# Performance work log

Hardware: AMD Instinct MI355X
Metric: run time of the kernel (lower is better)

Reference implementation:

```python
import jax, jax.numpy as jnp
import numpy as np

N = 100000
E = 1600000
D_IN = 128
D_HID = 128
D_OUT = 64


def mish(x):
    return x * jnp.tanh(jax.nn.softplus(x))


def sage_conv(x, src, dst, W_l, b_l, W_r):
    # gather source-node features along edges, mean-aggregate at destination
    msg = x[src]  # [E, d]
    agg = jax.ops.segment_sum(msg, dst, num_segments=N)  # [N, d]
    cnt = jax.ops.segment_sum(jnp.ones((E,), x.dtype), dst, num_segments=N)
    agg = agg / jnp.maximum(cnt, 1.0)[:, None]
    # PyG SAGEConv: lin_l(aggregated) + lin_r(root); lin_r has no bias
    return agg @ W_l.T + b_l + x @ W_r.T


def setup_inputs() -> dict:
    key = jax.random.key(0)
    ks = jax.random.split(key, 10)
    s = lambda d: 1.0 / np.sqrt(d)
    return {
        "x": jax.random.normal(ks[0], (N, D_IN), jnp.float32),
        "edge_index": jax.random.randint(ks[1], (2, E), 0, N, jnp.int64),
        "W_l0": jax.random.normal(ks[2], (D_HID, D_IN), jnp.float32) * s(D_IN),
        "b_l0": jnp.zeros((D_HID,), jnp.float32),
        "W_r0": jax.random.normal(ks[3], (D_HID, D_IN), jnp.float32) * s(D_IN),
        "W_l1": jax.random.normal(ks[4], (D_HID, D_HID), jnp.float32) * s(D_HID),
        "b_l1": jnp.zeros((D_HID,), jnp.float32),
        "W_r1": jax.random.normal(ks[5], (D_HID, D_HID), jnp.float32) * s(D_HID),
        "W_head": jax.random.normal(ks[6], (D_OUT, D_HID), jnp.float32) * s(D_HID),
        "b_head": jnp.zeros((D_OUT,), jnp.float32),
    }


def reference(x, edge_index, W_l0, b_l0, W_r0, W_l1, b_l1, W_r1, W_head, b_head):
    src, dst = edge_index[0], edge_index[1]
    h = mish(sage_conv(x, src, dst, W_l0, b_l0, W_r0))  # dropout is identity in eval
    h = mish(sage_conv(h, src, dst, W_l1, b_l1, W_r1))
    return h @ W_head.T + b_head
```

## Files before the change

### kernel.cpp

```cpp
#include <hip/hip_runtime.h>
#include <math.h>

#define N_NODES 100000
#define N_EDGES 1600000
#define DF      128
#define D_HEAD  64

#define NWIN    128
#define WIN_SZ  782
#define CAP     13312
#define BCH     8192

typedef __attribute__((ext_vector_type(8))) short bf16x8;
typedef __attribute__((ext_vector_type(4))) float f32x4;

static __device__ __forceinline__ float mish_f(float v) {
    float e = __expf(v);
    float q = 1.0f + e;
    float p = q * q;
    float m = v * (p - 1.0f) / (p + 1.0f);
    return (v > 40.0f) ? v : m;
}

static __device__ __forceinline__ unsigned short f2bf(float f) {
    unsigned int u = __builtin_bit_cast(unsigned int, f);
    unsigned int r = (u + 0x7fffu + ((u >> 16) & 1u)) >> 16;
    return (unsigned short)r;
}
static __device__ __forceinline__ float bf2f(unsigned int bits16) {
    return __builtin_bit_cast(float, bits16 << 16);
}


#define XB 12500
#define WB 288

__global__ void cvt_kernel(const float* __restrict__ x,
                           const float* __restrict__ Wl0, const float* __restrict__ Wr0,
                           const float* __restrict__ Wl1, const float* __restrict__ Wr1,
                           const float* __restrict__ Wh,
                           unsigned short* __restrict__ xb, unsigned short* __restrict__ wb,
                           int* __restrict__ bucket_cnt) {
    int b = blockIdx.x;
    if (b < XB) {
        int i = b * 256 + threadIdx.x;
        float4 v = ((const float4*)x)[i];
        ushort4 o;
        o.x = f2bf(v.x); o.y = f2bf(v.y); o.z = f2bf(v.z); o.w = f2bf(v.w);
        ((ushort4*)xb)[i] = o;
    } else if (b < XB + WB) {
        int id = (b - XB) * 256 + threadIdx.x;
        if (id < 65536) {
            int seg = id >> 14;
            int r   = id & 16383;
            const float* W = (seg == 0) ? Wl0 : (seg == 1) ? Wr0 : (seg == 2) ? Wl1 : Wr1;
            wb[id] = f2bf(W[r]);
        } else {
            wb[id] = f2bf(Wh[id - 65536]);
        }
    } else {
        if (threadIdx.x < NWIN) bucket_cnt[threadIdx.x] = 0;
    }
}


__global__ __launch_bounds__(256) void bucket_kernel(const int* __restrict__ src,
                                                     const int* __restrict__ dst,
                                                     int* __restrict__ bucket_cnt,
                                                     unsigned int* __restrict__ pairs) {
    __shared__ int cnt[NWIN];
    __shared__ int base[NWIN];
    int tid = threadIdx.x;
    int e0  = blockIdx.x * BCH;
    if (tid < NWIN) cnt[tid] = 0;
    __syncthreads();
    #pragma unroll 4
    for (int i = 0; i < BCH / 256; ++i) {
        int e = e0 + tid + i * 256;
        if (e < N_EDGES) atomicAdd(&cnt[dst[e] / WIN_SZ], 1);
    }
    __syncthreads();
    if (tid < NWIN) {
        base[tid] = atomicAdd(&bucket_cnt[tid], cnt[tid]);
        cnt[tid] = 0;
    }
    __syncthreads();
    #pragma unroll 4
    for (int i = 0; i < BCH / 256; ++i) {
        int e = e0 + tid + i * 256;
        if (e < N_EDGES) {
            int d  = dst[e];
            int s  = src[e];
            int w  = d / WIN_SZ;
            int dl = d - w * WIN_SZ;
            int p  = atomicAdd(&cnt[w], 1);
            int idx = base[w] + p;
            if (idx < CAP)
                pairs[(size_t)w * CAP + idx] = (unsigned)s | ((unsigned)dl << 17);
        }
    }
}


__global__ __launch_bounds__(256) void build_win(const unsigned int* __restrict__ pairs,
                                                 const int* __restrict__ bucket_cnt,
                                                 int* __restrict__ rowstart,
                                                 int* __restrict__ csr) {
    __shared__ int ldeg[WIN_SZ];
    __shared__ int lcsr[CAP];
    __shared__ int wsum[4];
    __shared__ int red[4];

    int tid = threadIdx.x;
    int w   = blockIdx.x;
    int base_node = w * WIN_SZ;
    int nn = N_NODES - base_node;
    if (nn > WIN_SZ) nn = WIN_SZ;
    if (nn < 0) nn = 0;

    for (int i = tid; i < WIN_SZ; i += 256) ldeg[i] = 0;

    int val = (tid < w) ? bucket_cnt[tid] : 0;
    #pragma unroll
    for (int o = 32; o; o >>= 1) val += __shfl_xor(val, o);
    if ((tid & 63) == 0) red[tid >> 6] = val;
    int n_pairs = bucket_cnt[w];
    if (n_pairs > CAP) n_pairs = CAP;
    __syncthreads();
    int ebase = red[0] + red[1] + red[2] + red[3];

    const unsigned int* pw = pairs + (size_t)w * CAP;

    for (int i = tid; i < n_pairs; i += 256)
        atomicAdd(&ldeg[pw[i] >> 17], 1);
    __syncthreads();

    int i0 = tid * 4;
    int v[4];
    int s = 0;
    #pragma unroll
    for (int q = 0; q < 4; ++q) {
        v[q] = (i0 + q < nn) ? ldeg[i0 + q] : 0;
        s += v[q];
    }
    int lane = tid & 63, wv = tid >> 6;
    int sc = s;
    #pragma unroll
    for (int d = 1; d < 64; d <<= 1) {
        int t = __shfl_up(sc, d);
        if (lane >= d) sc += t;
    }
    if (lane == 63) wsum[wv] = sc;
    __syncthreads();
    int woff = 0;
    for (int q = 0; q < wv; ++q) woff += wsum[q];
    int run = woff + sc - s;
    #pragma unroll
    for (int q = 0; q < 4; ++q) {
        if (i0 + q < nn) {
            rowstart[base_node + i0 + q] = ebase + run;
            ldeg[i0 + q] = run;
            run += v[q];
        }
    }
    if (w == NWIN - 1 && tid == 0) rowstart[N_NODES] = N_EDGES;
    __syncthreads();

    for (int i = tid; i < n_pairs; i += 256) {
        unsigned int p = pw[i];
        int slot = atomicAdd(&ldeg[p >> 17], 1);
        lcsr[slot] = (int)(p & 0x1FFFFu);
    }
    __syncthreads();

    for (int i = tid; i < n_pairs; i += 256)
        csr[ebase + i] = lcsr[i];
}


__global__ __launch_bounds__(256) void aggregate_kernel(const unsigned short* __restrict__ X,
                                                        const int* __restrict__ rowstart,
                                                        const int* __restrict__ csr,
                                                        unsigned short* __restrict__ out) {
    int wv   = threadIdx.x >> 6;
    int lane = threadIdx.x & 63;
    int node = blockIdx.x * 4 + wv;
    if (node >= N_NODES) return;
    int slot = lane >> 4;
    int l16  = lane & 15;
    int rs0 = rowstart[node];
    int rs1 = rowstart[node + 1];

    float acc[8];
    #pragma unroll
    for (int i = 0; i < 8; ++i) acc[i] = 0.f;

    for (int e0 = rs0; e0 < rs1; e0 += 16) {
        uint4 v[4];
        #pragma unroll
        for (int j = 0; j < 4; ++j) {
            int e = e0 + 4 * j + slot;
            uint4 t = {0u, 0u, 0u, 0u};
            if (e < rs1) t = *(const uint4*)(X + (size_t)csr[e] * DF + l16 * 8);
            v[j] = t;
        }
        #pragma unroll
        for (int j = 0; j < 4; ++j) {
            unsigned int w0[4] = {v[j].x, v[j].y, v[j].z, v[j].w};
            #pragma unroll
            for (int i = 0; i < 4; ++i) {
                acc[2 * i]     += bf2f(w0[i] & 0xffffu);
                acc[2 * i + 1] += bf2f(w0[i] >> 16);
            }
        }
    }

    #pragma unroll
    for (int i = 0; i < 8; ++i) {
        acc[i] += __shfl_xor(acc[i], 32);
        acc[i] += __shfl_xor(acc[i], 16);
    }

    int d = rs1 - rs0;
    float inv = 1.0f / (float)(d > 0 ? d : 1);
    if (slot == 0) {
        unsigned int r[4];
        #pragma unroll
        for (int i = 0; i < 4; ++i) {
            unsigned int lo = f2bf(acc[2 * i] * inv);
            unsigned int hi = f2bf(acc[2 * i + 1] * inv);
            r[i] = lo | (hi << 16);
        }
        uint4 o = {r[0], r[1], r[2], r[3]};
        *(uint4*)(out + (size_t)node * DF + l16 * 8) = o;
    }
}


template <int COLS, bool TWO, bool MISH, bool OUT_BF16>
__global__ __launch_bounds__(256) void mfma_gemm(const unsigned short* __restrict__ A,
                                                 const unsigned short* __restrict__ H,
                                                 const unsigned short* __restrict__ Wl,
                                                 const unsigned short* __restrict__ Wr,
                                                 const float* __restrict__ bias,
                                                 void* __restrict__ out, int M) {
    constexpr int NT  = COLS / 16;
    constexpr int LDA = 136;

    __shared__ unsigned short As[64 * LDA];
    __shared__ unsigned short Ws[COLS * LDA];

    int tid  = threadIdx.x;
    int wv   = tid >> 6;
    int lane = tid & 63;
    int quad = lane >> 4;
    int l16  = lane & 15;
    int m0   = blockIdx.x * 64;

    f32x4 acc[NT];
    #pragma unroll
    for (int n = 0; n < NT; ++n) acc[n] = (f32x4){0.f, 0.f, 0.f, 0.f};

    #pragma unroll
    for (int phase = 0; phase < (TWO ? 2 : 1); ++phase) {
        const unsigned short* Ain = phase ? H : A;
        const unsigned short* Win = phase ? Wr : Wl;
        __syncthreads();
        #pragma unroll
        for (int i = 0; i < COLS / 16; ++i) {
            int idx = tid + i * 256;
            int r   = idx >> 4;
            int cb  = (idx & 15) * 8;
            *(uint4*)&Ws[r * LDA + cb] = *(const uint4*)&Win[r * 128 + cb];
        }
        #pragma unroll
        for (int i = 0; i < 4; ++i) {
            int idx = tid + i * 256;
            int r   = idx >> 4;
            int cb  = (idx & 15) * 8;
            uint4 v = {0u, 0u, 0u, 0u};
            if (m0 + r < M) v = *(const uint4*)&Ain[(size_t)(m0 + r) * 128 + cb];
            *(uint4*)&As[r * LDA + cb] = v;
        }
        __syncthreads();
        #pragma unroll
        for (int ks = 0; ks < 4; ++ks) {
            bf16x8 af = *(const bf16x8*)&As[(wv * 16 + l16) * LDA + ks * 32 + quad * 8];
            #pragma unroll
            for (int n = 0; n < NT; ++n) {
                bf16x8 bfr = *(const bf16x8*)&Ws[(n * 16 + l16) * LDA + ks * 32 + quad * 8];
                acc[n] = __builtin_amdgcn_mfma_f32_16x16x32_bf16(af, bfr, acc[n], 0, 0, 0);
            }
        }
    }

    #pragma unroll
    for (int n = 0; n < NT; ++n) {
        int col = n * 16 + l16;
        float b = bias[col];
        #pragma unroll
        for (int r = 0; r < 4; ++r) {
            int row = m0 + wv * 16 + quad * 4 + r;
            if (row < M) {
                float v = acc[n][r] + b;
                if constexpr (MISH) v = mish_f(v);
                if constexpr (OUT_BF16)
                    ((unsigned short*)out)[(size_t)row * COLS + col] = f2bf(v);
                else
                    ((float*)out)[(size_t)row * COLS + col] = v;
            }
        }
    }
}


extern "C" void kernel_launch(void* const* d_in, const int* in_sizes, int n_in,
                              void* d_out, int out_size, void* d_ws, size_t ws_size,
                              hipStream_t stream) {
    const float* x   = (const float*)d_in[0];
    const int*   ei  = (const int*)d_in[1];
    const float* Wl0 = (const float*)d_in[2];
    const float* bl0 = (const float*)d_in[3];
    const float* Wr0 = (const float*)d_in[4];
    const float* Wl1 = (const float*)d_in[5];
    const float* bl1 = (const float*)d_in[6];
    const float* Wr1 = (const float*)d_in[7];
    const float* Wh  = (const float*)d_in[8];
    const float* bh  = (const float*)d_in[9];
    float* out = (float*)d_out;

    const int* src = ei;
    const int* dst = ei + N_EDGES;

    char* ws = (char*)d_ws;
    size_t off = 0;
    auto alloc = [&](size_t bytes) -> void* {
        void* p = ws + off;
        off += (bytes + 255) & ~(size_t)255;
        return p;
    };
    int* rowstart   = (int*)alloc((N_NODES + 1) * 4);
    int* csr        = (int*)alloc(N_EDGES * 4);
    int* bucket_cnt = (int*)alloc(NWIN * 4);

    unsigned short* Wb  = (unsigned short*)alloc((size_t)(65536 + 8192) * 2);
    unsigned short* Xb  = (unsigned short*)alloc((size_t)N_NODES * DF * 2);
    unsigned short* Ab  = (unsigned short*)alloc((size_t)N_NODES * DF * 2);
    unsigned short* H1b = (unsigned short*)alloc((size_t)N_NODES * DF * 2);

    unsigned short* Wlb0 = Wb;
    unsigned short* Wrb0 = Wb + 16384;
    unsigned short* Wlb1 = Wb + 32768;
    unsigned short* Wrb1 = Wb + 49152;
    unsigned short* Whb  = Wb + 65536;
    unsigned short* H2b  = Xb;
    unsigned int* pairs  = (unsigned int*)H1b;

    cvt_kernel<<<XB + WB + 1, 256, 0, stream>>>(x, Wl0, Wr0, Wl1, Wr1, Wh, Xb, Wb, bucket_cnt);

    bucket_kernel<<<(N_EDGES + BCH - 1) / BCH, 256, 0, stream>>>(src, dst, bucket_cnt, pairs);
    build_win<<<NWIN, 256, 0, stream>>>(pairs, bucket_cnt, rowstart, csr);

    const int gemm_grid = (N_NODES + 63) / 64;

    aggregate_kernel<<<N_NODES / 4, 256, 0, stream>>>(Xb, rowstart, csr, Ab);
    mfma_gemm<128, true, true, true><<<gemm_grid, 256, 0, stream>>>(
        Ab, Xb, Wlb0, Wrb0, bl0, H1b, N_NODES);
    aggregate_kernel<<<N_NODES / 4, 256, 0, stream>>>(H1b, rowstart, csr, Ab);
    mfma_gemm<128, true, true, true><<<gemm_grid, 256, 0, stream>>>(
        Ab, H1b, Wlb1, Wrb1, bl1, H2b, N_NODES);
    mfma_gemm<64, false, false, false><<<gemm_grid, 256, 0, stream>>>(
        H2b, nullptr, Whb, nullptr, bh, out, N_NODES);
}
```

Measured before the change: 381.0 us.

## Fuse neighbor aggregation into SAGE GEMM and split bucket atomics

Each wave now mean-aggregates its 16 destination nodes straight into shared memory. It then runs the Wl MFMA from there, reloads the root rows into the same tile for the Wr MFMA, and applies bias and mish in the same kernel. This removes the separate aggregation kernel and the global write and read of the aggregated matrix for both layers. Weights are now read from global/cache rather than staged in LDS, and each wave walks its nodes one after another. The edge-bucketing kernel also spreads each window counter over 4 per-lane-set sub-counters to cut shared-memory atomic contention.

```diff
diff --git a/kernel.cpp b/kernel.cpp
--- a/kernel.cpp
+++ b/kernel.cpp
@@ -68,21 +68,26 @@
                                                      const int* __restrict__ dst,
                                                      int* __restrict__ bucket_cnt,
                                                      unsigned int* __restrict__ pairs) {
-    __shared__ int cnt[NWIN];
-    __shared__ int base[NWIN];
+    __shared__ int cnt[NWIN][4];
+    __shared__ int cur[NWIN][4];
     int tid = threadIdx.x;
+    int set = tid & 3;
     int e0  = blockIdx.x * BCH;
-    if (tid < NWIN) cnt[tid] = 0;
+    for (int i = tid; i < NWIN * 4; i += 256) ((int*)cnt)[i] = 0;
     __syncthreads();
     #pragma unroll 4
     for (int i = 0; i < BCH / 256; ++i) {
         int e = e0 + tid + i * 256;
-        if (e < N_EDGES) atomicAdd(&cnt[dst[e] / WIN_SZ], 1);
+        if (e < N_EDGES) atomicAdd(&cnt[dst[e] / WIN_SZ][set], 1);
     }
     __syncthreads();
     if (tid < NWIN) {
-        base[tid] = atomicAdd(&bucket_cnt[tid], cnt[tid]);
-        cnt[tid] = 0;
+        int c0 = cnt[tid][0], c1 = cnt[tid][1], c2 = cnt[tid][2], c3 = cnt[tid][3];
+        int b = atomicAdd(&bucket_cnt[tid], c0 + c1 + c2 + c3);
+        cur[tid][0] = b;
+        cur[tid][1] = b + c0;
+        cur[tid][2] = b + c0 + c1;
+        cur[tid][3] = b + c0 + c1 + c2;
     }
     __syncthreads();
     #pragma unroll 4
@@ -93,8 +98,7 @@
             int s  = src[e];
             int w  = d / WIN_SZ;
             int dl = d - w * WIN_SZ;
-            int p  = atomicAdd(&cnt[w], 1);
-            int idx = base[w] + p;
+            int idx = atomicAdd(&cur[w][set], 1);
             if (idx < CAP)
                 pairs[(size_t)w * CAP + idx] = (unsigned)s | ((unsigned)dl << 17);
         }
@@ -178,77 +182,15 @@
 }
 
 
-__global__ __launch_bounds__(256) void aggregate_kernel(const unsigned short* __restrict__ X,
-                                                        const int* __restrict__ rowstart,
-                                                        const int* __restrict__ csr,
-                                                        unsigned short* __restrict__ out) {
-    int wv   = threadIdx.x >> 6;
-    int lane = threadIdx.x & 63;
-    int node = blockIdx.x * 4 + wv;
-    if (node >= N_NODES) return;
-    int slot = lane >> 4;
-    int l16  = lane & 15;
-    int rs0 = rowstart[node];
-    int rs1 = rowstart[node + 1];
-
-    float acc[8];
-    #pragma unroll
-    for (int i = 0; i < 8; ++i) acc[i] = 0.f;
-
-    for (int e0 = rs0; e0 < rs1; e0 += 16) {
-        uint4 v[4];
-        #pragma unroll
-        for (int j = 0; j < 4; ++j) {
-            int e = e0 + 4 * j + slot;
-            uint4 t = {0u, 0u, 0u, 0u};
-            if (e < rs1) t = *(const uint4*)(X + (size_t)csr[e] * DF + l16 * 8);
-            v[j] = t;
-        }
-        #pragma unroll
-        for (int j = 0; j < 4; ++j) {
-            unsigned int w0[4] = {v[j].x, v[j].y, v[j].z, v[j].w};
-            #pragma unroll
-            for (int i = 0; i < 4; ++i) {
-                acc[2 * i]     += bf2f(w0[i] & 0xffffu);
-                acc[2 * i + 1] += bf2f(w0[i] >> 16);
-            }
-        }
-    }
-
-    #pragma unroll
-    for (int i = 0; i < 8; ++i) {
-        acc[i] += __shfl_xor(acc[i], 32);
-        acc[i] += __shfl_xor(acc[i], 16);
-    }
-
-    int d = rs1 - rs0;
-    float inv = 1.0f / (float)(d > 0 ? d : 1);
-    if (slot == 0) {
-        unsigned int r[4];
-        #pragma unroll
-        for (int i = 0; i < 4; ++i) {
-            unsigned int lo = f2bf(acc[2 * i] * inv);
-            unsigned int hi = f2bf(acc[2 * i + 1] * inv);
-            r[i] = lo | (hi << 16);
-        }
-        uint4 o = {r[0], r[1], r[2], r[3]};
-        *(uint4*)(out + (size_t)node * DF + l16 * 8) = o;
-    }
-}
-
-
-template <int COLS, bool TWO, bool MISH, bool OUT_BF16>
-__global__ __launch_bounds__(256) void mfma_gemm(const unsigned short* __restrict__ A,
-                                                 const unsigned short* __restrict__ H,
-                                                 const unsigned short* __restrict__ Wl,
-                                                 const unsigned short* __restrict__ Wr,
-                                                 const float* __restrict__ bias,
-                                                 void* __restrict__ out, int M) {
-    constexpr int NT  = COLS / 16;
+__global__ __launch_bounds__(256, 4) void fused_sage(const unsigned short* __restrict__ X,
+                                                     const int* __restrict__ rowstart,
+                                                     const int* __restrict__ csr,
+                                                     const unsigned short* __restrict__ Wl,
+                                                     const unsigned short* __restrict__ Wr,
+                                                     const float* __restrict__ bias,
+                                                     unsigned short* __restrict__ out) {
     constexpr int LDA = 136;
-
     __shared__ unsigned short As[64 * LDA];
-    __shared__ unsigned short Ws[COLS * LDA];
 
     int tid  = threadIdx.x;
     int wv   = tid >> 6;
@@ -257,58 +199,147 @@
     int l16  = lane & 15;
     int m0   = blockIdx.x * 64;
 
-    f32x4 acc[NT];
-    #pragma unroll
-    for (int n = 0; n < NT; ++n) acc[n] = (f32x4){0.f, 0.f, 0.f, 0.f};
-
-    #pragma unroll
-    for (int phase = 0; phase < (TWO ? 2 : 1); ++phase) {
-        const unsigned short* Ain = phase ? H : A;
-        const unsigned short* Win = phase ? Wr : Wl;
-        __syncthreads();
-        #pragma unroll
-        for (int i = 0; i < COLS / 16; ++i) {
-            int idx = tid + i * 256;
-            int r   = idx >> 4;
-            int cb  = (idx & 15) * 8;
-            *(uint4*)&Ws[r * LDA + cb] = *(const uint4*)&Win[r * 128 + cb];
-        }
-        #pragma unroll
-        for (int i = 0; i < 4; ++i) {
-            int idx = tid + i * 256;
-            int r   = idx >> 4;
-            int cb  = (idx & 15) * 8;
-            uint4 v = {0u, 0u, 0u, 0u};
-            if (m0 + r < M) v = *(const uint4*)&Ain[(size_t)(m0 + r) * 128 + cb];
-            *(uint4*)&As[r * LDA + cb] = v;
-        }
-        __syncthreads();
-        #pragma unroll
-        for (int ks = 0; ks < 4; ++ks) {
-            bf16x8 af = *(const bf16x8*)&As[(wv * 16 + l16) * LDA + ks * 32 + quad * 8];
+    for (int n = 0; n < 16; ++n) {
+        int node = m0 + wv * 16 + n;
+        float acc[8];
+        #pragma unroll
+        for (int i = 0; i < 8; ++i) acc[i] = 0.f;
+        int rs0 = 0, rs1 = 0;
+        if (node < N_NODES) { rs0 = rowstart[node]; rs1 = rowstart[node + 1]; }
+        for (int e0 = rs0; e0 < rs1; e0 += 16) {
+            uint4 v[4];
             #pragma unroll
-            for (int n = 0; n < NT; ++n) {
-                bf16x8 bfr = *(const bf16x8*)&Ws[(n * 16 + l16) * LDA + ks * 32 + quad * 8];
-                acc[n] = __builtin_amdgcn_mfma_f32_16x16x32_bf16(af, bfr, acc[n], 0, 0, 0);
+            for (int j = 0; j < 4; ++j) {
+                int e = e0 + 4 * j + quad;
+                uint4 t = {0u, 0u, 0u, 0u};
+                if (e < rs1) t = *(const uint4*)(X + (size_t)csr[e] * DF + l16 * 8);
+                v[j] = t;
             }
-        }
-    }
-
-    #pragma unroll
-    for (int n = 0; n < NT; ++n) {
+            #pragma unroll
+            for (int j = 0; j < 4; ++j) {
+                unsigned int w0[4] = {v[j].x, v[j].y, v[j].z, v[j].w};
+                #pragma unroll
+                for (int i = 0; i < 4; ++i) {
+                    acc[2 * i]     += bf2f(w0[i] & 0xffffu);
+                    acc[2 * i + 1] += bf2f(w0[i] >> 16);
+                }
+            }
+        }
+        #pragma unroll
+        for (int i = 0; i < 8; ++i) {
+            acc[i] += __shfl_xor(acc[i], 32);
+            acc[i] += __shfl_xor(acc[i], 16);
+        }
+        if (quad == 0) {
+            int dcnt = rs1 - rs0;
+            float inv = 1.0f / (float)(dcnt > 0 ? dcnt : 1);
+            unsigned int r[4];
+            #pragma unroll
+            for (int i = 0; i < 4; ++i) {
+                unsigned int lo = f2bf(acc[2 * i] * inv);
+                unsigned int hi = f2bf(acc[2 * i + 1] * inv);
+                r[i] = lo | (hi << 16);
+            }
+            uint4 o = {r[0], r[1], r[2], r[3]};
+            *(uint4*)&As[(wv * 16 + n) * LDA + l16 * 8] = o;
+        }
+    }
+
+    f32x4 acc[8];
+    #pragma unroll
+    for (int n = 0; n < 8; ++n) acc[n] = (f32x4){0.f, 0.f, 0.f, 0.f};
+    #pragma unroll
+    for (int ks = 0; ks < 4; ++ks) {
+        bf16x8 af = *(const bf16x8*)&As[(wv * 16 + l16) * LDA + ks * 32 + quad * 8];
+        #pragma unroll
+        for (int n = 0; n < 8; ++n) {
+            bf16x8 bfr = *(const bf16x8*)&Wl[(n * 16 + l16) * 128 + ks * 32 + quad * 8];
+            acc[n] = __builtin_amdgcn_mfma_f32_16x16x32_bf16(af, bfr, acc[n], 0, 0, 0);
+        }
+    }
+
+    #pragma unroll
+    for (int i = 0; i < 4; ++i) {
+        int o   = i * 1024 + lane * 16;
+        int row = o >> 8;
+        int col = o & 255;
+        int gr  = m0 + wv * 16 + row;
+        if (gr > N_NODES - 1) gr = N_NODES - 1;
+        uint4 t = *(const uint4*)((const char*)X + (size_t)gr * 256 + col);
+        *(uint4*)((char*)As + (size_t)(wv * 16 + row) * (LDA * 2) + col) = t;
+    }
+
+    #pragma unroll
+    for (int ks = 0; ks < 4; ++ks) {
+        bf16x8 af = *(const bf16x8*)&As[(wv * 16 + l16) * LDA + ks * 32 + quad * 8];
+        #pragma unroll
+        for (int n = 0; n < 8; ++n) {
+            bf16x8 bfr = *(const bf16x8*)&Wr[(n * 16 + l16) * 128 + ks * 32 + quad * 8];
+            acc[n] = __builtin_amdgcn_mfma_f32_16x16x32_bf16(af, bfr, acc[n], 0, 0, 0);
+        }
+    }
+
+    #pragma unroll
+    for (int n = 0; n < 8; ++n) {
         int col = n * 16 + l16;
         float b = bias[col];
         #pragma unroll
         for (int r = 0; r < 4; ++r) {
             int row = m0 + wv * 16 + quad * 4 + r;
-            if (row < M) {
-                float v = acc[n][r] + b;
-                if constexpr (MISH) v = mish_f(v);
-                if constexpr (OUT_BF16)
-                    ((unsigned short*)out)[(size_t)row * COLS + col] = f2bf(v);
-                else
-                    ((float*)out)[(size_t)row * COLS + col] = v;
+            if (row < N_NODES) {
+                float v = mish_f(acc[n][r] + b);
+                out[(size_t)row * 128 + col] = f2bf(v);
             }
+        }
+    }
+}
+
+
+__global__ __launch_bounds__(256, 4) void head_gemm(const unsigned short* __restrict__ H,
+                                                    const unsigned short* __restrict__ Wh,
+                                                    const float* __restrict__ bias,
+                                                    float* __restrict__ out) {
+    constexpr int LDA = 136;
+    __shared__ unsigned short As[64 * LDA];
+    int tid  = threadIdx.x;
+    int wv   = tid >> 6;
+    int lane = tid & 63;
+    int quad = lane >> 4;
+    int l16  = lane & 15;
+    int m0   = blockIdx.x * 64;
+
+    #pragma unroll
+    for (int i = 0; i < 4; ++i) {
+        int o   = i * 1024 + lane * 16;
+        int row = o >> 8;
+        int col = o & 255;
+        int gr  = m0 + wv * 16 + row;
+        if (gr > N_NODES - 1) gr = N_NODES - 1;
+        uint4 t = *(const uint4*)((const char*)H + (size_t)gr * 256 + col);
+        *(uint4*)((char*)As + (size_t)(wv * 16 + row) * (LDA * 2) + col) = t;
+    }
+
+    f32x4 acc[4];
+    #pragma unroll
+    for (int n = 0; n < 4; ++n) acc[n] = (f32x4){0.f, 0.f, 0.f, 0.f};
+    #pragma unroll
+    for (int ks = 0; ks < 4; ++ks) {
+        bf16x8 af = *(const bf16x8*)&As[(wv * 16 + l16) * LDA + ks * 32 + quad * 8];
+        #pragma unroll
+        for (int n = 0; n < 4; ++n) {
+            bf16x8 bfr = *(const bf16x8*)&Wh[(n * 16 + l16) * 128 + ks * 32 + quad * 8];
+            acc[n] = __builtin_amdgcn_mfma_f32_16x16x32_bf16(af, bfr, acc[n], 0, 0, 0);
+        }
+    }
+
+    #pragma unroll
+    for (int n = 0; n < 4; ++n) {
+        int col = n * 16 + l16;
+        float b = bias[col];
+        #pragma unroll
+        for (int r = 0; r < 4; ++r) {
+            int row = m0 + wv * 16 + quad * 4 + r;
+            if (row < N_NODES) out[(size_t)row * 64 + col] = acc[n][r] + b;
         }
     }
 }
@@ -345,7 +376,6 @@
 
     unsigned short* Wb  = (unsigned short*)alloc((size_t)(65536 + 8192) * 2);
     unsigned short* Xb  = (unsigned short*)alloc((size_t)N_NODES * DF * 2);
-    unsigned short* Ab  = (unsigned short*)alloc((size_t)N_NODES * DF * 2);
     unsigned short* H1b = (unsigned short*)alloc((size_t)N_NODES * DF * 2);
 
     unsigned short* Wlb0 = Wb;
@@ -361,14 +391,9 @@
     bucket_kernel<<<(N_EDGES + BCH - 1) / BCH, 256, 0, stream>>>(src, dst, bucket_cnt, pairs);
     build_win<<<NWIN, 256, 0, stream>>>(pairs, bucket_cnt, rowstart, csr);
 
-    const int gemm_grid = (N_NODES + 63) / 64;
-
-    aggregate_kernel<<<N_NODES / 4, 256, 0, stream>>>(Xb, rowstart, csr, Ab);
-    mfma_gemm<128, true, true, true><<<gemm_grid, 256, 0, stream>>>(
-        Ab, Xb, Wlb0, Wrb0, bl0, H1b, N_NODES);
-    aggregate_kernel<<<N_NODES / 4, 256, 0, stream>>>(H1b, rowstart, csr, Ab);
-    mfma_gemm<128, true, true, true><<<gemm_grid, 256, 0, stream>>>(
-        Ab, H1b, Wlb1, Wrb1, bl1, H2b, N_NODES);
-    mfma_gemm<64, false, false, false><<<gemm_grid, 256, 0, stream>>>(
-        H2b, nullptr, Whb, nullptr, bh, out, N_NODES);
-}
+    const int grid = (N_NODES + 63) / 64;
+
+    fused_sage<<<grid, 256, 0, stream>>>(Xb,  rowstart, csr, Wlb0, Wrb0, bl0, H1b);
+    fused_sage<<<grid, 256, 0, stream>>>(H1b, rowstart, csr, Wlb1, Wrb1, bl1, H2b);
+    head_gemm<<<grid, 256, 0, stream>>>(H2b, Whb, bh, out);
+}
```

New measurement: 496.5 us. 1.3x slower.

## Load GEMM operands directly from global memory and split bucket counters by lane set

Applied to the files above, without the earlier changes.

The GEMM kernels no longer stage activations and weights through shared memory. Each wave loads its A fragments and its weight fragments straight from global memory, which removes the LDS round trips and the block barriers, raises the occupancy hint, and clamps tail rows instead of zero-filling them. The bucketing kernel spreads its shared-memory counters over four sub-counters per window to cut atomic contention, and it keeps the dst values in registers so dst is not read twice. The cost is that weight fragments are now re-read from global memory or cache by every wave.

```diff
diff --git a/kernel.cpp b/kernel.cpp
--- a/kernel.cpp
+++ b/kernel.cpp
@@ -68,33 +68,41 @@
                                                      const int* __restrict__ dst,
                                                      int* __restrict__ bucket_cnt,
                                                      unsigned int* __restrict__ pairs) {
-    __shared__ int cnt[NWIN];
-    __shared__ int base[NWIN];
+    __shared__ int cnt[NWIN][4];
+    __shared__ int cur[NWIN][4];
     int tid = threadIdx.x;
+    int set = tid & 3;
     int e0  = blockIdx.x * BCH;
-    if (tid < NWIN) cnt[tid] = 0;
-    __syncthreads();
+    for (int i = tid; i < NWIN * 4; i += 256) ((int*)cnt)[i] = 0;
+    __syncthreads();
+
+    int dc[BCH / 256];
     #pragma unroll 4
     for (int i = 0; i < BCH / 256; ++i) {
         int e = e0 + tid + i * 256;
-        if (e < N_EDGES) atomicAdd(&cnt[dst[e] / WIN_SZ], 1);
+        int d = (e < N_EDGES) ? dst[e] : -1;
+        dc[i] = d;
+        if (d >= 0) atomicAdd(&cnt[d / WIN_SZ][set], 1);
     }
     __syncthreads();
     if (tid < NWIN) {
-        base[tid] = atomicAdd(&bucket_cnt[tid], cnt[tid]);
-        cnt[tid] = 0;
+        int c0 = cnt[tid][0], c1 = cnt[tid][1], c2 = cnt[tid][2], c3 = cnt[tid][3];
+        int b = atomicAdd(&bucket_cnt[tid], c0 + c1 + c2 + c3);
+        cur[tid][0] = b;
+        cur[tid][1] = b + c0;
+        cur[tid][2] = b + c0 + c1;
+        cur[tid][3] = b + c0 + c1 + c2;
     }
     __syncthreads();
     #pragma unroll 4
     for (int i = 0; i < BCH / 256; ++i) {
-        int e = e0 + tid + i * 256;
-        if (e < N_EDGES) {
-            int d  = dst[e];
+        int d = dc[i];
+        if (d >= 0) {
+            int e  = e0 + tid + i * 256;
             int s  = src[e];
             int w  = d / WIN_SZ;
             int dl = d - w * WIN_SZ;
-            int p  = atomicAdd(&cnt[w], 1);
-            int idx = base[w] + p;
+            int idx = atomicAdd(&cur[w][set], 1);
             if (idx < CAP)
                 pairs[(size_t)w * CAP + idx] = (unsigned)s | ((unsigned)dl << 17);
         }
@@ -238,18 +246,13 @@
 
 
 template <int COLS, bool TWO, bool MISH, bool OUT_BF16>
-__global__ __launch_bounds__(256) void mfma_gemm(const unsigned short* __restrict__ A,
-                                                 const unsigned short* __restrict__ H,
-                                                 const unsigned short* __restrict__ Wl,
-                                                 const unsigned short* __restrict__ Wr,
-                                                 const float* __restrict__ bias,
-                                                 void* __restrict__ out, int M) {
-    constexpr int NT  = COLS / 16;
-    constexpr int LDA = 136;
-
-    __shared__ unsigned short As[64 * LDA];
-    __shared__ unsigned short Ws[COLS * LDA];
-
+__global__ __launch_bounds__(256, 4) void sage_gemm(const unsigned short* __restrict__ A,
+                                                    const unsigned short* __restrict__ H,
+                                                    const unsigned short* __restrict__ Wl,
+                                                    const unsigned short* __restrict__ Wr,
+                                                    const float* __restrict__ bias,
+                                                    void* __restrict__ out) {
+    constexpr int NT = COLS / 16;
     int tid  = threadIdx.x;
     int wv   = tid >> 6;
     int lane = tid & 63;
@@ -257,38 +260,31 @@
     int l16  = lane & 15;
     int m0   = blockIdx.x * 64;
 
+    int arow = m0 + wv * 16 + l16;
+    if (arow > N_NODES - 1) arow = N_NODES - 1;
+
     f32x4 acc[NT];
     #pragma unroll
     for (int n = 0; n < NT; ++n) acc[n] = (f32x4){0.f, 0.f, 0.f, 0.f};
 
-    #pragma unroll
-    for (int phase = 0; phase < (TWO ? 2 : 1); ++phase) {
-        const unsigned short* Ain = phase ? H : A;
-        const unsigned short* Win = phase ? Wr : Wl;
-        __syncthreads();
-        #pragma unroll
-        for (int i = 0; i < COLS / 16; ++i) {
-            int idx = tid + i * 256;
-            int r   = idx >> 4;
-            int cb  = (idx & 15) * 8;
-            *(uint4*)&Ws[r * LDA + cb] = *(const uint4*)&Win[r * 128 + cb];
-        }
-        #pragma unroll
-        for (int i = 0; i < 4; ++i) {
-            int idx = tid + i * 256;
-            int r   = idx >> 4;
-            int cb  = (idx & 15) * 8;
-            uint4 v = {0u, 0u, 0u, 0u};
-            if (m0 + r < M) v = *(const uint4*)&Ain[(size_t)(m0 + r) * 128 + cb];
-            *(uint4*)&As[r * LDA + cb] = v;
-        }
-        __syncthreads();
+    const unsigned short* Ap = A + (size_t)arow * 128 + quad * 8;
+    #pragma unroll
+    for (int ks = 0; ks < 4; ++ks) {
+        bf16x8 af = *(const bf16x8*)(Ap + ks * 32);
+        #pragma unroll
+        for (int n = 0; n < NT; ++n) {
+            bf16x8 bfr = *(const bf16x8*)&Wl[(n * 16 + l16) * 128 + ks * 32 + quad * 8];
+            acc[n] = __builtin_amdgcn_mfma_f32_16x16x32_bf16(af, bfr, acc[n], 0, 0, 0);
+        }
+    }
+    if constexpr (TWO) {
+        const unsigned short* Hp = H + (size_t)arow * 128 + quad * 8;
         #pragma unroll
         for (int ks = 0; ks < 4; ++ks) {
-            bf16x8 af = *(const bf16x8*)&As[(wv * 16 + l16) * LDA + ks * 32 + quad * 8];
+            bf16x8 af = *(const bf16x8*)(Hp + ks * 32);
             #pragma unroll
             for (int n = 0; n < NT; ++n) {
-                bf16x8 bfr = *(const bf16x8*)&Ws[(n * 16 + l16) * LDA + ks * 32 + quad * 8];
+                bf16x8 bfr = *(const bf16x8*)&Wr[(n * 16 + l16) * 128 + ks * 32 + quad * 8];
                 acc[n] = __builtin_amdgcn_mfma_f32_16x16x32_bf16(af, bfr, acc[n], 0, 0, 0);
             }
         }
@@ -301,7 +297,7 @@
         #pragma unroll
         for (int r = 0; r < 4; ++r) {
             int row = m0 + wv * 16 + quad * 4 + r;
-            if (row < M) {
+            if (row < N_NODES) {
                 float v = acc[n][r] + b;
                 if constexpr (MISH) v = mish_f(v);
                 if constexpr (OUT_BF16)
@@ -361,14 +357,11 @@
     bucket_kernel<<<(N_EDGES + BCH - 1) / BCH, 256, 0, stream>>>(src, dst, bucket_cnt, pairs);
     build_win<<<NWIN, 256, 0, stream>>>(pairs, bucket_cnt, rowstart, csr);
 
-    const int gemm_grid = (N_NODES + 63) / 64;
+    const int grid = (N_NODES + 63) / 64;
 
     aggregate_kernel<<<N_NODES / 4, 256, 0, stream>>>(Xb, rowstart, csr, Ab);
-    mfma_gemm<128, true, true, true><<<gemm_grid, 256, 0, stream>>>(
-        Ab, Xb, Wlb0, Wrb0, bl0, H1b, N_NODES);
+    sage_gemm<128, true, true, true><<<grid, 256, 0, stream>>>(Ab, Xb, Wlb0, Wrb0, bl0, H1b);
     aggregate_kernel<<<N_NODES / 4, 256, 0, stream>>>(H1b, rowstart, csr, Ab);
-    mfma_gemm<128, true, true, true><<<gemm_grid, 256, 0, stream>>>(
-        Ab, H1b, Wlb1, Wrb1, bl1, H2b, N_NODES);
-    mfma_gemm<64, false, false, false><<<gemm_grid, 256, 0, stream>>>(
-        H2b, nullptr, Whb, nullptr, bh, out, N_NODES);
-}
+    sage_gemm<128, true, true, true><<<grid, 256, 0, stream>>>(Ab, H1b, Wlb1, Wrb1, bl1, H2b);
+    sage_gemm<64, false, false, false><<<grid, 256, 0, stream>>>(H2b, nullptr, Whb, nullptr, bh, out);
+}
```

Result: slower. 447.3 us (+17.4%).
